# Optimization experiments

Hardware: AMD Instinct MI355X
Metric: run time of the kernel (lower is better)

## Reference

```python
import jax, jax.numpy as jnp
import numpy as np

D = 64          # embedding_dim
B = 1024        # batch (queries)
R = 128         # num_relations
N = 100000      # num_nodes
E = 6400000     # num_edges


def setup_inputs() -> dict:
    key = jax.random.key(0)
    ks = jax.random.split(key, 16)
    inp = {
        "relation_embeddings": jax.random.normal(ks[0], (B, R, D), dtype=jnp.float32),
        "query_rels": jax.random.randint(ks[1], (B,), 0, R),
        "query_entities": jax.random.randint(ks[2], (B,), 0, N),
        "edge_index": jax.random.randint(ks[3], (2, E), 0, N),
        "edge_type": jax.random.randint(ks[4], (E,), 0, R),
        "num_nodes": N,
        # feature_extractor: Linear(2D+4 -> D), ReLU, Linear(D -> D//2), ReLU
        "W1": jax.random.normal(ks[5], (2 * D + 4, D), dtype=jnp.float32) * 0.05,
        "b1": jnp.zeros((D,), dtype=jnp.float32),
        "W2": jax.random.normal(ks[6], (D, D // 2), dtype=jnp.float32) * 0.05,
        "b2": jnp.zeros((D // 2,), dtype=jnp.float32),
        # gate_network: Linear(D//2 -> D//4), ReLU, Linear(D//4 -> 1), Sigmoid
        "Wg1": jax.random.normal(ks[7], (D // 2, D // 4), dtype=jnp.float32) * 0.05,
        "bg1": jnp.zeros((D // 4,), dtype=jnp.float32),
        "Wg2": jax.random.normal(ks[8], (D // 4, 1), dtype=jnp.float32) * 0.05,
        "bg2": jnp.full((1,), 0.85, dtype=jnp.float32),
    }
    return inp


def reference(relation_embeddings, query_rels, query_entities, edge_index,
              edge_type, num_nodes, W1, b1, W2, b2, Wg1, bg1, Wg2, bg2):
    b, r, d = relation_embeddings.shape
    e = edge_type.shape[0]
    e_f = jnp.float32(e)
    src, dst = edge_index[0], edge_index[1]
    # count self-loop edges once (matches boolean OR mask in torch code)
    not_loop = (src != dst).astype(jnp.float32)

    # --- graph statistics (vectorized replacement of per-query masks) ---
    rel_counts = jnp.zeros((r,), jnp.float32).at[edge_type].add(1.0)          # [R]
    rel_freq_norm = jnp.minimum(rel_counts[query_rels] / e_f, 1.0)            # [B]

    deg = (jnp.zeros((num_nodes,), jnp.float32)
           .at[src].add(1.0).at[dst].add(not_loop))                           # [N]
    deg_q = deg[query_entities]                                               # [B]
    entity_degree_norm = jnp.minimum(deg_q / e_f, 1.0)

    density = jnp.minimum(e_f / jnp.float32(num_nodes * num_nodes), 1.0)
    stats = jnp.stack([rel_freq_norm, entity_degree_norm, rel_freq_norm,
                       jnp.full_like(rel_freq_norm, density)], axis=-1)       # [B,4]

    # --- query relation embedding ---
    rel_emb = relation_embeddings[jnp.arange(b), query_rels]                  # [B,D]

    # --- entity embedding = mean of relation embeddings over incident edges ---
    # per-node histogram of incident edge types (self loops counted once)
    hist = (jnp.zeros((num_nodes, r), jnp.float32)
            .at[src, edge_type].add(1.0)
            .at[dst, edge_type].add(not_loop))                                # [N,R]
    Mq = hist[query_entities]                                                 # [B,R]
    ent_sum = jnp.einsum('br,brd->bd', Mq, relation_embeddings)               # [B,D]
    entity_emb = ent_sum / jnp.maximum(deg_q, 1.0)[:, None]                   # zeros if deg==0

    # --- gated MLP ---
    feat = jnp.concatenate([rel_emb, entity_emb, stats], axis=-1)             # [B,2D+4]
    h = jax.nn.relu(feat @ W1 + b1)
    h = jax.nn.relu(h @ W2 + b2)
    g = jax.nn.relu(h @ Wg1 + bg1)
    gate = jax.nn.sigmoid(g @ Wg2 + bg2)[:, 0]                                # [B]
    return gate
```

## Files before the change

### kernel.cpp

```cpp
#include <hip/hip_runtime.h>
#include <math.h>


#define NNODES 100000
#define NWORDS ((NNODES + 31) / 32)
#define NWP    (((NWORDS + 3) / 4) * 4)
#define RR     128
#define DD     64
#define FF     (2 * DD + 4)
#define E4C    1600000
#define EDGE_BLOCKS 2048
#define EDGE_THREADS 256
#define NTC    (EDGE_BLOCKS * EDGE_THREADS)
#define HITCAP 512
#define SETUP_BLOCKS 256
#define NHIST  (SETUP_BLOCKS - 1)

__global__ void __launch_bounds__(1024)
setup_kernel(const int* __restrict__ qents, int B,
             unsigned* __restrict__ gmask, int* __restrict__ gbase,
             const int* __restrict__ etype, int E,
             int* __restrict__ relpart, int4* __restrict__ mz, int mz4)
{
    int t = threadIdx.x;
    if (blockIdx.x != 0) {
        __shared__ int s_cnt[RR];
        if (t < RR) s_cnt[t] = 0;
        __syncthreads();
        int zi = (blockIdx.x - 1) * 1024 + t;
        if (zi < mz4) mz[zi] = make_int4(0, 0, 0, 0);
        int ne4 = E >> 2;
        const int4* et4 = (const int4*)etype;
        int i = (blockIdx.x - 1) * 1024 + t;
        int stride = NHIST * 1024;
        for (int k = i; k < ne4; k += stride) {
            int4 ty = et4[k];
            atomicAdd(&s_cnt[ty.x], 1);
            atomicAdd(&s_cnt[ty.y], 1);
            atomicAdd(&s_cnt[ty.z], 1);
            atomicAdd(&s_cnt[ty.w], 1);
        }
        if (blockIdx.x == 1) {
            for (int e = (ne4 << 2) + t; e < E; e += 1024)
                atomicAdd(&s_cnt[etype[e]], 1);
        }
        __syncthreads();
        if (t < RR) relpart[(blockIdx.x - 1) * RR + t] = s_cnt[t];
        return;
    }
    __shared__ unsigned s_mask[NWP];
    __shared__ int s_wsum[16], s_wbase[16];
    for (int k = t; k < NWP; k += 1024) s_mask[k] = 0u;
    __syncthreads();
    for (int b = t; b < B; b += 1024) {
        int e = qents[b];
        atomicOr(&s_mask[e >> 5], 1u << (e & 31));
    }
    __syncthreads();
    int w0 = t * 4;
    int pc[4]; int sum = 0;
#pragma unroll
    for (int k = 0; k < 4; ++k) {
        int w = w0 + k;
        unsigned mm = (w < NWP) ? s_mask[w] : 0u;
        pc[k] = __popc(mm);
        sum += pc[k];
    }
    int lane = t & 63, wid = t >> 6;
    int incl = sum;
#pragma unroll
    for (int off = 1; off < 64; off <<= 1) {
        int v = __shfl_up(incl, off);
        if (lane >= off) incl += v;
    }
    if (lane == 63) s_wsum[wid] = incl;
    __syncthreads();
    if (t == 0) {
        int run = 0;
#pragma unroll
        for (int k = 0; k < 16; ++k) { s_wbase[k] = run; run += s_wsum[k]; }
    }
    __syncthreads();
    int base = s_wbase[wid] + incl - sum;
#pragma unroll
    for (int k = 0; k < 4; ++k) {
        int w = w0 + k;
        if (w < NWP) gbase[w] = base;
        base += pc[k];
    }
    for (int k = t; k < NWP; k += 1024) gmask[k] = s_mask[k];
}

static __device__ __forceinline__ void hitrec(
    int node, int e,
    const unsigned* s_mask, const int* __restrict__ gbase,
    unsigned* s_hnode, unsigned* s_hedge, int* s_hn,
    int* __restrict__ Mslot, const int* __restrict__ etype)
{
    unsigned w = s_mask[node >> 5];
    if ((w >> (node & 31)) & 1u) {
        int idx = atomicAdd(s_hn, 1);
        if (idx < HITCAP) {
            s_hnode[idx] = (unsigned)node;
            s_hedge[idx] = (unsigned)e;
        } else {
            int slot = gbase[node >> 5] + __popc(w & ((1u << (node & 31)) - 1u));
            atomicAdd(&Mslot[slot * RR + etype[e]], 1);
        }
    }
}

static __device__ __forceinline__ void edge4s(
    int4 s, int4 d, int i,
    const unsigned* s_mask, const int* __restrict__ gbase,
    unsigned* s_hnode, unsigned* s_hedge, int* s_hn,
    int* __restrict__ Mslot, const int* __restrict__ etype)
{
    int e = i * 4;
    hitrec(s.x, e + 0, s_mask, gbase, s_hnode, s_hedge, s_hn, Mslot, etype);
    if (s.x != d.x) hitrec(d.x, e + 0, s_mask, gbase, s_hnode, s_hedge, s_hn, Mslot, etype);
    hitrec(s.y, e + 1, s_mask, gbase, s_hnode, s_hedge, s_hn, Mslot, etype);
    if (s.y != d.y) hitrec(d.y, e + 1, s_mask, gbase, s_hnode, s_hedge, s_hn, Mslot, etype);
    hitrec(s.z, e + 2, s_mask, gbase, s_hnode, s_hedge, s_hn, Mslot, etype);
    if (s.z != d.z) hitrec(d.z, e + 2, s_mask, gbase, s_hnode, s_hedge, s_hn, Mslot, etype);
    hitrec(s.w, e + 3, s_mask, gbase, s_hnode, s_hedge, s_hn, Mslot, etype);
    if (s.w != d.w) hitrec(d.w, e + 3, s_mask, gbase, s_hnode, s_hedge, s_hn, Mslot, etype);
}

__global__ void __launch_bounds__(EDGE_THREADS, 8)
edge_kernel(const int* __restrict__ ei, const int* __restrict__ etype,
            int E, int E4,
            const unsigned* __restrict__ gmask, const int* __restrict__ gbase,
            int* __restrict__ Mslot,
            const int* __restrict__ relpart, int* __restrict__ relcnt)
{
    __shared__ __align__(16) unsigned s_mask[NWP];
    __shared__ unsigned s_hnode[HITCAP];
    __shared__ unsigned s_hedge[HITCAP];
    __shared__ int s_hn;
    int t = threadIdx.x;
    if (t == 0) s_hn = 0;

    if (blockIdx.x == 0 && t < RR) {
        int sum = 0;
        for (int i = 0; i < NHIST; ++i) sum += relpart[i * RR + t];
        relcnt[t] = sum;
    }

    const uint4* gm4 = (const uint4*)gmask;
    for (int i = t; i < NWP / 4; i += EDGE_THREADS)
        ((uint4*)s_mask)[i] = gm4[i];
    __syncthreads();

    int tid  = blockIdx.x * EDGE_THREADS + t;
    int nthr = gridDim.x * EDGE_THREADS;

    const int4* src4 = (const int4*)ei;
    const int4* dst4 = (const int4*)(ei + E);

    if (E4 == E4C && nthr == NTC) {
        int i0 = tid, i1 = tid + NTC, i2 = tid + 2 * NTC, i3 = tid + 3 * NTC;
        int4 s0 = src4[i0], d0 = dst4[i0];
        int4 s1 = src4[i1], d1 = dst4[i1];
        edge4s(s0, d0, i0, s_mask, gbase, s_hnode, s_hedge, &s_hn, Mslot, etype);
        int4 s2 = src4[i2], d2 = dst4[i2];
        edge4s(s1, d1, i1, s_mask, gbase, s_hnode, s_hedge, &s_hn, Mslot, etype);
        bool has3 = (i3 < E4C);
        int4 s3, d3;
        if (has3) { s3 = src4[i3]; d3 = dst4[i3]; }
        edge4s(s2, d2, i2, s_mask, gbase, s_hnode, s_hedge, &s_hn, Mslot, etype);
        if (has3)
            edge4s(s3, d3, i3, s_mask, gbase, s_hnode, s_hedge, &s_hn, Mslot, etype);
    } else {
        for (int i = tid; i < E4; i += nthr) {
            int4 s = src4[i], d = dst4[i];
            edge4s(s, d, i, s_mask, gbase, s_hnode, s_hedge, &s_hn, Mslot, etype);
        }
        for (int e = (E4 << 2) + tid; e < E; e += nthr) {
            int s = ei[e], d = ei[E + e];
            hitrec(s, e, s_mask, gbase, s_hnode, s_hedge, &s_hn, Mslot, etype);
            if (s != d)
                hitrec(d, e, s_mask, gbase, s_hnode, s_hedge, &s_hn, Mslot, etype);
        }
    }

    __syncthreads();
    int hn = s_hn; if (hn > HITCAP) hn = HITCAP;
    for (int i = t; i < hn; i += EDGE_THREADS) {
        int node = (int)s_hnode[i];
        int e    = (int)s_hedge[i];
        unsigned w = s_mask[node >> 5];
        int slot = gbase[node >> 5] + __popc(w & ((1u << (node & 31)) - 1u));
        atomicAdd(&Mslot[slot * RR + etype[e]], 1);
    }
}

__global__ void query_kernel(
    const float* __restrict__ RE,
    const int* __restrict__ qrels, const int* __restrict__ qents,
    const int* __restrict__ relcnt, const int* __restrict__ Mslot,
    const unsigned* __restrict__ gmask, const int* __restrict__ gbase,
    const float* __restrict__ W1, const float* __restrict__ b1,
    const float* __restrict__ W2, const float* __restrict__ b2,
    const float* __restrict__ Wg1, const float* __restrict__ bg1,
    const float* __restrict__ Wg2, const float* __restrict__ bg2,
    float* __restrict__ out, float e_f, float density)
{
    __shared__ float s_m[RR];
    __shared__ float s_part[256];
    __shared__ float s_feat[FF];
    __shared__ float s_h1[DD];
    __shared__ float s_h2[DD / 2];
    __shared__ float s_g[DD / 4];
    __shared__ int s_slot;

    int b = blockIdx.x;
    int t = threadIdx.x;
    int d = t & (DD - 1);
    int w = t >> 6;

    if (t == 0) {
        int e = qents[b];
        unsigned mm = gmask[e >> 5];
        s_slot = gbase[e >> 5] + __popc(mm & ((1u << (e & 31)) - 1u));
    }
    __syncthreads();
    int slot = s_slot;

    if (t < RR) s_m[t] = (float)Mslot[slot * RR + t];
    __syncthreads();

    const float* REb = RE + (size_t)b * RR * DD;
    float acc = 0.f;
#pragma unroll 8
    for (int r = w; r < RR; r += 4)
        acc = fmaf(s_m[r], REb[r * DD + d], acc);
    s_part[w * DD + d] = acc;
    __syncthreads();

    if (t < DD) {
        float ds = s_m[t] + s_m[t + DD];
#pragma unroll
        for (int off = 32; off > 0; off >>= 1) ds += __shfl_xor(ds, off);

        float ent = s_part[t] + s_part[DD + t] + s_part[2 * DD + t] + s_part[3 * DD + t];

        int qr = qrels[b];
        s_feat[t]      = REb[qr * DD + t];
        s_feat[DD + t] = ent / fmaxf(ds, 1.f);
        if (t == 0) {
            float rf = fminf((float)relcnt[qr] / e_f, 1.f);
            s_feat[2 * DD + 0] = rf;
            s_feat[2 * DD + 1] = fminf(ds / e_f, 1.f);
            s_feat[2 * DD + 2] = rf;
            s_feat[2 * DD + 3] = density;
        }
    }
    __syncthreads();

    {
        int c = t >> 6, n = t & 63;
        int i0 = c * 33;
        float a = 0.f;
#pragma unroll
        for (int k = 0; k < 33; ++k) {
            int i = i0 + k;
            a = fmaf(s_feat[i], W1[i * DD + n], a);
        }
        s_part[t] = a;
    }
    __syncthreads();
    if (t < DD) {
        float a = b1[t] + s_part[t] + s_part[64 + t] + s_part[128 + t] + s_part[192 + t];
        s_h1[t] = fmaxf(a, 0.f);
    }
    __syncthreads();

    {
        int c = t >> 5, n = t & 31;
        float a = 0.f;
#pragma unroll
        for (int k = 0; k < 8; ++k) {
            int i = c * 8 + k;
            a = fmaf(s_h1[i], W2[i * 32 + n], a);
        }
        s_part[t] = a;
    }
    __syncthreads();
    if (t < 32) {
        float a = b2[t];
#pragma unroll
        for (int c = 0; c < 8; ++c) a += s_part[c * 32 + t];
        s_h2[t] = fmaxf(a, 0.f);
    }
    __syncthreads();

    if (t < 16) {
        float a = bg1[t];
#pragma unroll
        for (int i = 0; i < 32; ++i) a = fmaf(s_h2[i], Wg1[i * 16 + t], a);
        s_g[t] = fmaxf(a, 0.f);
    }
    __syncthreads();

    if (t == 0) {
        float a = bg2[0];
#pragma unroll
        for (int i = 0; i < 16; ++i) a = fmaf(s_g[i], Wg2[i], a);
        out[b] = 1.f / (1.f + expf(-a));
    }
}

extern "C" void kernel_launch(void* const* d_in, const int* in_sizes, int n_in,
                              void* d_out, int out_size, void* d_ws, size_t ws_size,
                              hipStream_t stream)
{
    const float* RE    = (const float*)d_in[0];
    const int*   qrels = (const int*)d_in[1];
    const int*   qents = (const int*)d_in[2];
    const int*   ei    = (const int*)d_in[3];
    const int*   etype = (const int*)d_in[4];
    const float* W1  = (const float*)d_in[6];
    const float* b1  = (const float*)d_in[7];
    const float* W2  = (const float*)d_in[8];
    const float* b2  = (const float*)d_in[9];
    const float* Wg1 = (const float*)d_in[10];
    const float* bg1 = (const float*)d_in[11];
    const float* Wg2 = (const float*)d_in[12];
    const float* bg2 = (const float*)d_in[13];
    float* out = (float*)d_out;

    int B = in_sizes[1];
    int E = in_sizes[4];

    int* ws_i   = (int*)d_ws;
    int* Mslot  = ws_i;
    int* relcnt = Mslot + (size_t)B * RR;
    unsigned* mask = (unsigned*)(relcnt + RR);
    int* word_base = (int*)(mask + NWP);
    int* relpart   = word_base + NWP;

    float e_f = (float)E;
    float density = fminf((float)E / ((float)NNODES * (float)NNODES), 1.f);

    int mz4 = (B * RR) / 4;

    setup_kernel<<<SETUP_BLOCKS, 1024, 0, stream>>>(qents, B, mask, word_base,
                                                    etype, E, relpart,
                                                    (int4*)Mslot, mz4);

    int E4 = ((E & 3) == 0) ? (E >> 2) : 0;
    edge_kernel<<<EDGE_BLOCKS, EDGE_THREADS, 0, stream>>>(ei, etype, E, E4,
                                                          mask, word_base, Mslot,
                                                          relpart, relcnt);

    query_kernel<<<B, 256, 0, stream>>>(RE, qrels, qents, relcnt, Mslot,
                                        mask, word_base,
                                        W1, b1, W2, b2, Wg1, bg1, Wg2, bg2,
                                        out, e_f, density);
}
```

Measured before the change: 46.50 us.

## Split zeroing into dedicated blocks, privatize histogram, reorder edge loads, skip zero-count rows

The setup kernel now gives zeroing of the slot matrix its own 64 blocks, and spreads the relation histogram over four per-wavefront-group copies in shared memory to cut atomic contention. The remaining blocks do the histogram and their partial sums are merged. The edge kernel issues three int4 src/dst loads before processing them to expose more memory-level parallelism, with the fourth chunk loaded afterward. The final einsum skips loading relation-embedding rows whose histogram count is zero, which saves bandwidth but adds a data-dependent branch.

Result: no change. 46.85 us (+0.7%).

```diff
diff --git a/kernel.cpp b/kernel.cpp
--- a/kernel.cpp
+++ b/kernel.cpp
@@ -14,7 +14,8 @@
 #define NTC    (EDGE_BLOCKS * EDGE_THREADS)
 #define HITCAP 512
 #define SETUP_BLOCKS 256
-#define NHIST  (SETUP_BLOCKS - 1)
+#define ZBLOCKS 64
+#define NHIST  (SETUP_BLOCKS - 1 - ZBLOCKS)
 
 __global__ void __launch_bounds__(1024)
 setup_kernel(const int* __restrict__ qents, int B,
@@ -23,29 +24,38 @@
              int* __restrict__ relpart, int4* __restrict__ mz, int mz4)
 {
     int t = threadIdx.x;
-    if (blockIdx.x != 0) {
-        __shared__ int s_cnt[RR];
-        if (t < RR) s_cnt[t] = 0;
+    int bid = blockIdx.x;
+    if (bid >= 1 && bid <= ZBLOCKS) {
+        int zi = (bid - 1) * 1024 + t;
+        if (zi < mz4) mz[zi] = make_int4(0, 0, 0, 0);
+        return;
+    }
+    if (bid > ZBLOCKS) {
+        __shared__ int s_cnt[4][RR];
+        int wid = t >> 6;
+        int sub = wid & 3;
+        if (t < 4 * RR) ((int*)s_cnt)[t] = 0;
         __syncthreads();
-        int zi = (blockIdx.x - 1) * 1024 + t;
-        if (zi < mz4) mz[zi] = make_int4(0, 0, 0, 0);
+        int hb = bid - ZBLOCKS - 1;
         int ne4 = E >> 2;
         const int4* et4 = (const int4*)etype;
-        int i = (blockIdx.x - 1) * 1024 + t;
+        int i = hb * 1024 + t;
         int stride = NHIST * 1024;
         for (int k = i; k < ne4; k += stride) {
             int4 ty = et4[k];
-            atomicAdd(&s_cnt[ty.x], 1);
-            atomicAdd(&s_cnt[ty.y], 1);
-            atomicAdd(&s_cnt[ty.z], 1);
-            atomicAdd(&s_cnt[ty.w], 1);
-        }
-        if (blockIdx.x == 1) {
+            atomicAdd(&s_cnt[sub][ty.x], 1);
+            atomicAdd(&s_cnt[sub][ty.y], 1);
+            atomicAdd(&s_cnt[sub][ty.z], 1);
+            atomicAdd(&s_cnt[sub][ty.w], 1);
+        }
+        if (hb == 0) {
             for (int e = (ne4 << 2) + t; e < E; e += 1024)
-                atomicAdd(&s_cnt[etype[e]], 1);
+                atomicAdd(&s_cnt[sub][etype[e]], 1);
         }
         __syncthreads();
-        if (t < RR) relpart[(blockIdx.x - 1) * RR + t] = s_cnt[t];
+        if (t < RR)
+            relpart[hb * RR + t] = s_cnt[0][t] + s_cnt[1][t]
+                                 + s_cnt[2][t] + s_cnt[3][t];
         return;
     }
     __shared__ unsigned s_mask[NWP];
@@ -159,18 +169,18 @@
     const int4* dst4 = (const int4*)(ei + E);
 
     if (E4 == E4C && nthr == NTC) {
-        int i0 = tid, i1 = tid + NTC, i2 = tid + 2 * NTC, i3 = tid + 3 * NTC;
-        int4 s0 = src4[i0], d0 = dst4[i0];
-        int4 s1 = src4[i1], d1 = dst4[i1];
-        edge4s(s0, d0, i0, s_mask, gbase, s_hnode, s_hedge, &s_hn, Mslot, etype);
-        int4 s2 = src4[i2], d2 = dst4[i2];
-        edge4s(s1, d1, i1, s_mask, gbase, s_hnode, s_hedge, &s_hn, Mslot, etype);
-        bool has3 = (i3 < E4C);
-        int4 s3, d3;
-        if (has3) { s3 = src4[i3]; d3 = dst4[i3]; }
-        edge4s(s2, d2, i2, s_mask, gbase, s_hnode, s_hedge, &s_hn, Mslot, etype);
-        if (has3)
-            edge4s(s3, d3, i3, s_mask, gbase, s_hnode, s_hedge, &s_hn, Mslot, etype);
+        int i0 = tid, i1 = tid + NTC, i2 = tid + 2 * NTC;
+        int4 sa = src4[i0], da = dst4[i0];
+        int4 sb = src4[i1], db = dst4[i1];
+        int4 sc = src4[i2], dc = dst4[i2];
+        edge4s(sa, da, i0, s_mask, gbase, s_hnode, s_hedge, &s_hn, Mslot, etype);
+        edge4s(sb, db, i1, s_mask, gbase, s_hnode, s_hedge, &s_hn, Mslot, etype);
+        edge4s(sc, dc, i2, s_mask, gbase, s_hnode, s_hedge, &s_hn, Mslot, etype);
+        int i3 = tid + 3 * NTC;
+        if (i3 < E4C) {
+            int4 sd = src4[i3], dd = dst4[i3];
+            edge4s(sd, dd, i3, s_mask, gbase, s_hnode, s_hedge, &s_hn, Mslot, etype);
+        }
     } else {
         for (int i = tid; i < E4; i += nthr) {
             int4 s = src4[i], d = dst4[i];
@@ -232,9 +242,11 @@
 
     const float* REb = RE + (size_t)b * RR * DD;
     float acc = 0.f;
-#pragma unroll 8
-    for (int r = w; r < RR; r += 4)
-        acc = fmaf(s_m[r], REb[r * DD + d], acc);
+#pragma unroll 4
+    for (int r = w; r < RR; r += 4) {
+        float m = s_m[r];
+        if (m != 0.f) acc = fmaf(m, REb[r * DD + d], acc);
+    }
     s_part[w * DD + d] = acc;
     __syncthreads();
 
```
